# Performance work log

Measured on AMD Instinct MI355X. Metric: run time of the kernel, lower is better.

## Reference

```python
import jax, jax.numpy as jnp
import numpy as np

T, N, D = 4096, 32768, 1024

def setup_inputs() -> dict:
    key = jax.random.key(0)
    k1, k2 = jax.random.split(key)
    x = jax.random.normal(k1, (T, D), dtype=jnp.float32)
    embeddings = jax.random.normal(k2, (N, D), dtype=jnp.float32)
    return {"x": x, "embeddings": embeddings}

def reference(x, embeddings):
    # scores: [T, N] = x @ E^T (unscaled single-head attention, Q=x, K=V=E)
    scores = jnp.einsum('td,nd->tn', x, embeddings)
    probs = jax.nn.softmax(scores, axis=-1)
    # out: [T, D] = probs @ E
    return jnp.einsum('tn,nd->td', probs, embeddings)
```

## Files before the change

kernel.cpp:

```cpp
#include <hip/hip_runtime.h>
#include <stdint.h>

#define T_DIM 4096
#define N_DIM 32768
#define D_DIM 1024
#define QB 64
#define KB 32
#define KSPLIT 4
#define ITERS (N_DIM / KSPLIT / KB)
#define NKB_TOT (N_DIM / KB)

typedef _Float16 f16;
typedef _Float16 f16x8 __attribute__((ext_vector_type(8)));
typedef _Float16 f16x4 __attribute__((ext_vector_type(4)));
typedef float f32x4 __attribute__((ext_vector_type(4)));

#define SWZ(q, k0) ((k0) ^ ((((q) >> 2) & 3) << 2))

struct __align__(16) Lds {
  float Spart[8][64][40];
  f16   P[64][40];
  float srow[64];
};

__global__ void e16_build(const float* __restrict__ E, f16* __restrict__ E16) {
  size_t i8 = (size_t)(blockIdx.x * 256 + threadIdx.x) * 8;
  float4 a = *(const float4*)(E + i8);
  float4 b = *(const float4*)(E + i8 + 4);
  f16x8 v = {(f16)a.x,(f16)a.y,(f16)a.z,(f16)a.w,
             (f16)b.x,(f16)b.y,(f16)b.z,(f16)b.w};
  *(f16x8*)(E16 + i8) = v;
}

__global__ void w2_build(const float* __restrict__ E, f16* __restrict__ W2) {
  int kb = blockIdx.x >> 2;
  int dg = blockIdx.x & 3;
  int d  = dg * 256 + threadIdx.x;
  for (int kq = 0; kq < 4; ++kq) {
    int k0 = kq * 8;
    f16x8 v;
    #pragma unroll
    for (int j = 0; j < 8; ++j)
      v[j] = (f16)E[(size_t)(kb*32 + k0 + j) * D_DIM + d];
    *(f16x8*)(W2 + (size_t)kb * (D_DIM*KB) + (size_t)d*KB + k0) = v;
  }
}

template<int USE_E16>
__global__ __launch_bounds__(512, 2)
void cboe_attn(const float* __restrict__ X, const float* __restrict__ Eg,
               const f16* __restrict__ E16, const f16* __restrict__ W2,
               f16* __restrict__ O16, float* __restrict__ ML)
{
  extern __shared__ char smem_raw[];
  Lds& L = *reinterpret_cast<Lds*>(smem_raw);
  const int tid   = threadIdx.x;
  const int lane  = tid & 63;
  const int w     = tid >> 6;
  const int c     = lane & 15;
  const int g     = lane >> 4;
  const int wd    = w * 128;
  const int qtile = blockIdx.x & 63;
  const int ks    = blockIdx.x >> 6;
  const int qb    = qtile * QB;
  const size_t key0 = (size_t)ks * (N_DIM / KSPLIT);
  const int sq    = tid >> 3;
  const int kslot = tid & 7;

  f16x8 qf[4][4];
  #pragma unroll
  for (int qt = 0; qt < 4; ++qt) {
    const float* qrow = X + (size_t)(qb + qt*16 + c) * D_DIM + wd;
    #pragma unroll
    for (int kc = 0; kc < 4; ++kc) {
      float4 a = *(const float4*)(qrow + kc*32 + g*8);
      float4 b = *(const float4*)(qrow + kc*32 + g*8 + 4);
      qf[qt][kc] = (f16x8){(f16)a.x,(f16)a.y,(f16)a.z,(f16)a.w,
                           (f16)b.x,(f16)b.y,(f16)b.z,(f16)b.w};
    }
  }

  f32x4 acc[4][8];
  #pragma unroll
  for (int qt = 0; qt < 4; ++qt)
    #pragma unroll
    for (int dt = 0; dt < 8; ++dt) acc[qt][dt] = (f32x4){0.f,0.f,0.f,0.f};

  float m_run = -1.0e30f, l_run = 0.0f;

  for (int it = 0; it < ITERS; ++it) {
    const size_t kb_glob = (size_t)ks * ITERS + it;
    const size_t kbase   = key0 + (size_t)it * KB;

    #pragma unroll
    for (int kt = 0; kt < 2; ++kt) {
      const size_t key = kbase + kt*16 + c;
      f16x8 ak[4];
      #pragma unroll
      for (int kc = 0; kc < 4; ++kc) {
        if (USE_E16) {
          ak[kc] = *(const f16x8*)(E16 + key*D_DIM + wd + kc*32 + g*8);
        } else {
          const float* p = Eg + key*D_DIM + wd + kc*32 + g*8;
          float4 a = *(const float4*)p;
          float4 b = *(const float4*)(p + 4);
          ak[kc] = (f16x8){(f16)a.x,(f16)a.y,(f16)a.z,(f16)a.w,
                           (f16)b.x,(f16)b.y,(f16)b.z,(f16)b.w};
        }
      }
      f32x4 sacc[4];
      #pragma unroll
      for (int qt = 0; qt < 4; ++qt) sacc[qt] = (f32x4){0.f,0.f,0.f,0.f};
      #pragma unroll
      for (int kc = 0; kc < 4; ++kc)
        #pragma unroll
        for (int qt = 0; qt < 4; ++qt)
          sacc[qt] = __builtin_amdgcn_mfma_f32_16x16x32_f16(ak[kc], qf[qt][kc], sacc[qt], 0, 0, 0);
      #pragma unroll
      for (int qt = 0; qt < 4; ++qt) {
        int q = qt*16 + c;
        *(f32x4*)&L.Spart[w][q][SWZ(q, kt*16 + g*4)] = sacc[qt];
      }
    }
    __syncthreads();

    f32x4 sv = (f32x4){0.f,0.f,0.f,0.f};
    #pragma unroll
    for (int w8 = 0; w8 < 8; ++w8)
      sv += *(const f32x4*)&L.Spart[w8][sq][SWZ(sq, kslot*4)];
    float tm = fmaxf(fmaxf(sv[0], sv[1]), fmaxf(sv[2], sv[3]));
    tm = fmaxf(tm, __shfl_xor(tm, 1));
    tm = fmaxf(tm, __shfl_xor(tm, 2));
    tm = fmaxf(tm, __shfl_xor(tm, 4));
    float mn = fmaxf(m_run, tm);
    float scale = __expf(m_run - mn);
    float p0 = __expf(sv[0] - mn), p1 = __expf(sv[1] - mn);
    float p2 = __expf(sv[2] - mn), p3 = __expf(sv[3] - mn);
    float psum = (p0 + p1) + (p2 + p3);
    psum += __shfl_xor(psum, 1);
    psum += __shfl_xor(psum, 2);
    psum += __shfl_xor(psum, 4);
    l_run = l_run * scale + psum;
    m_run = mn;
    *(f16x4*)&L.P[sq][kslot*4] = (f16x4){(f16)p0,(f16)p1,(f16)p2,(f16)p3};
    if (kslot == 0) L.srow[sq] = scale;
    __syncthreads();

    #pragma unroll
    for (int qt = 0; qt < 4; ++qt) {
      f32x4 sc = *(const f32x4*)&L.srow[qt*16 + g*4];
      #pragma unroll
      for (int dt = 0; dt < 8; ++dt) {
        acc[qt][dt][0] *= sc[0]; acc[qt][dt][1] *= sc[1];
        acc[qt][dt][2] *= sc[2]; acc[qt][dt][3] *= sc[3];
      }
    }
    f16x8 ap[4];
    #pragma unroll
    for (int qt = 0; qt < 4; ++qt)
      ap[qt] = *(const f16x8*)&L.P[qt*16 + c][g*8];
    const f16* vbase = W2 + kb_glob * (D_DIM*KB);
    #pragma unroll
    for (int dt = 0; dt < 8; ++dt) {
      f16x8 bv = *(const f16x8*)(vbase + (size_t)(wd + dt*16 + c)*KB + g*8);
      #pragma unroll
      for (int qt = 0; qt < 4; ++qt)
        acc[qt][dt] = __builtin_amdgcn_mfma_f32_16x16x32_f16(ap[qt], bv, acc[qt][dt], 0, 0, 0);
    }
  }

  if (kslot == 0) {
    size_t qg = (size_t)qb + sq;
    ML[((size_t)ks * T_DIM + qg) * 2 + 0] = m_run;
    ML[((size_t)ks * T_DIM + qg) * 2 + 1] = l_run;
  }
  #pragma unroll
  for (int qt = 0; qt < 4; ++qt)
    #pragma unroll
    for (int dt = 0; dt < 8; ++dt)
      #pragma unroll
      for (int r = 0; r < 4; ++r)
        O16[((size_t)ks * T_DIM + qb + qt*16 + 4*g + r) * D_DIM + wd + dt*16 + c] =
            (f16)acc[qt][dt][r];
}

__global__ void combine(const f16* __restrict__ O16, const float* __restrict__ ML,
                        float* __restrict__ Out) {
  int q  = blockIdx.x;
  int d0 = threadIdx.x * 4;
  float m[KSPLIT], l[KSPLIT];
  float M = -1.0e30f;
  #pragma unroll
  for (int ks = 0; ks < KSPLIT; ++ks) {
    m[ks] = ML[((size_t)ks * T_DIM + q) * 2 + 0];
    l[ks] = ML[((size_t)ks * T_DIM + q) * 2 + 1];
    M = fmaxf(M, m[ks]);
  }
  float Lsum = 0.f, wk[KSPLIT];
  #pragma unroll
  for (int ks = 0; ks < KSPLIT; ++ks) {
    wk[ks] = __expf(m[ks] - M);
    Lsum += l[ks] * wk[ks];
  }
  float inv = 1.0f / Lsum;
  float o0 = 0.f, o1 = 0.f, o2 = 0.f, o3 = 0.f;
  #pragma unroll
  for (int ks = 0; ks < KSPLIT; ++ks) {
    f16x4 v = *(const f16x4*)(O16 + ((size_t)ks * T_DIM + q) * D_DIM + d0);
    o0 += wk[ks] * (float)v[0];
    o1 += wk[ks] * (float)v[1];
    o2 += wk[ks] * (float)v[2];
    o3 += wk[ks] * (float)v[3];
  }
  float4 o = {o0 * inv, o1 * inv, o2 * inv, o3 * inv};
  *(float4*)(Out + (size_t)q * D_DIM + d0) = o;
}

extern "C" void kernel_launch(void* const* d_in, const int* in_sizes, int n_in,
                              void* d_out, int out_size, void* d_ws, size_t ws_size,
                              hipStream_t stream) {
  const float* X  = (const float*)d_in[0];
  const float* Eg = (const float*)d_in[1];
  float* Out = (float*)d_out;

  const size_t szE16 = (size_t)N_DIM * D_DIM * sizeof(f16);
  const size_t szW2  = (size_t)NKB_TOT * D_DIM * KB * sizeof(f16);
  const size_t szO16 = (size_t)KSPLIT * T_DIM * D_DIM * sizeof(f16);
  const size_t szML  = (size_t)KSPLIT * T_DIM * 2 * sizeof(float);
  const size_t needT1 = szE16 + szW2 + szO16 + szML;
  const int use_e16 = (d_ws && ws_size >= needT1) ? 1 : 0;

  char* p = (char*)d_ws;
  f16* E16 = nullptr;
  if (use_e16) { E16 = (f16*)p; p += szE16; }
  f16*   W2  = (f16*)p;   p += szW2;
  f16*   O16 = (f16*)p;   p += szO16;
  float* ML  = (float*)p;

  w2_build<<<dim3(NKB_TOT * 4), dim3(256), 0, stream>>>(Eg, W2);
  if (use_e16)
    e16_build<<<dim3((N_DIM * D_DIM) / (256 * 8)), dim3(256), 0, stream>>>(Eg, E16);

  const int shmem = (int)sizeof(Lds);
  if (use_e16) {
    hipFuncSetAttribute(reinterpret_cast<const void*>(&cboe_attn<1>),
                        hipFuncAttributeMaxDynamicSharedMemorySize, shmem);
    cboe_attn<1><<<dim3((T_DIM / QB) * KSPLIT), dim3(512), shmem, stream>>>(
        X, Eg, E16, W2, O16, ML);
  } else {
    hipFuncSetAttribute(reinterpret_cast<const void*>(&cboe_attn<0>),
                        hipFuncAttributeMaxDynamicSharedMemorySize, shmem);
    cboe_attn<0><<<dim3((T_DIM / QB) * KSPLIT), dim3(512), shmem, stream>>>(
        X, Eg, nullptr, W2, O16, ML);
  }
  combine<<<dim3(T_DIM), dim3(256), 0, stream>>>(O16, ML, Out);
}
```

Baseline: 1.835 ms.

## Use 1024-thread blocks with split query/D warps and lazy softmax rescaling

The attention kernel now runs 16 warps per block, with each warp covering half the query rows and a 64-wide slice of D, so each warp holds half the accumulators and Q fragments. The online softmax only raises the running max when it grows by more than 8, and the accumulator rescale is skipped when no row changed. Each partial output is normalised by its own l before writing, and combine is adjusted to match. A naive fp32 fallback kernel replaces the template for small workspaces. Together these aim to cut register pressure and per-iteration exp/multiply work, at the cost of more warps sharing each barrier and some fp16 range risk from the lazy max.

```diff
diff --git a/kernel.cpp b/kernel.cpp
--- a/kernel.cpp
+++ b/kernel.cpp
@@ -13,7 +13,9 @@
 typedef _Float16 f16;
 typedef _Float16 f16x8 __attribute__((ext_vector_type(8)));
 typedef _Float16 f16x4 __attribute__((ext_vector_type(4)));
+typedef _Float16 f16x2 __attribute__((ext_vector_type(2)));
 typedef float f32x4 __attribute__((ext_vector_type(4)));
+typedef float f32x2 __attribute__((ext_vector_type(2)));
 
 #define SWZ(q, k0) ((k0) ^ ((((q) >> 2) & 3) << 2))
 
@@ -21,6 +23,7 @@
   float Spart[8][64][40];
   f16   P[64][40];
   float srow[64];
+  float linv[64];
 };
 
 __global__ void e16_build(const float* __restrict__ E, f16* __restrict__ E16) {
@@ -46,142 +49,139 @@
   }
 }
 
-template<int USE_E16>
-__global__ __launch_bounds__(512, 2)
-void cboe_attn(const float* __restrict__ X, const float* __restrict__ Eg,
-               const f16* __restrict__ E16, const f16* __restrict__ W2,
-               f16* __restrict__ O16, float* __restrict__ ML)
+__global__ __launch_bounds__(1024)
+void cboe_attn(const float* __restrict__ X, const f16* __restrict__ E16,
+               const f16* __restrict__ W2, f16* __restrict__ O16,
+               float* __restrict__ ML)
 {
   extern __shared__ char smem_raw[];
   Lds& L = *reinterpret_cast<Lds*>(smem_raw);
-  const int tid   = threadIdx.x;
-  const int lane  = tid & 63;
-  const int w     = tid >> 6;
-  const int c     = lane & 15;
-  const int g     = lane >> 4;
-  const int wd    = w * 128;
+  const int tid  = threadIdx.x;
+  const int lane = tid & 63;
+  const int w    = tid >> 6;
+  const int c    = lane & 15;
+  const int g    = lane >> 4;
+  const int dq   = w & 7;
+  const int qh   = w >> 3;
+  const int wd   = w * 64;
   const int qtile = blockIdx.x & 63;
   const int ks    = blockIdx.x >> 6;
   const int qb    = qtile * QB;
   const size_t key0 = (size_t)ks * (N_DIM / KSPLIT);
-  const int sq    = tid >> 3;
-  const int kslot = tid & 7;
-
-  f16x8 qf[4][4];
-  #pragma unroll
-  for (int qt = 0; qt < 4; ++qt) {
-    const float* qrow = X + (size_t)(qb + qt*16 + c) * D_DIM + wd;
+  const int sq   = tid >> 4;
+  const int kp   = tid & 15;
+
+  f16x8 qf[2][4];
+  #pragma unroll
+  for (int j = 0; j < 2; ++j) {
+    const float* qrow = X + (size_t)(qb + (qh*2 + j)*16 + c) * D_DIM + dq*128;
     #pragma unroll
     for (int kc = 0; kc < 4; ++kc) {
       float4 a = *(const float4*)(qrow + kc*32 + g*8);
       float4 b = *(const float4*)(qrow + kc*32 + g*8 + 4);
-      qf[qt][kc] = (f16x8){(f16)a.x,(f16)a.y,(f16)a.z,(f16)a.w,
-                           (f16)b.x,(f16)b.y,(f16)b.z,(f16)b.w};
-    }
-  }
-
-  f32x4 acc[4][8];
+      qf[j][kc] = (f16x8){(f16)a.x,(f16)a.y,(f16)a.z,(f16)a.w,
+                          (f16)b.x,(f16)b.y,(f16)b.z,(f16)b.w};
+    }
+  }
+
+  f32x4 acc[4][4];
   #pragma unroll
   for (int qt = 0; qt < 4; ++qt)
     #pragma unroll
-    for (int dt = 0; dt < 8; ++dt) acc[qt][dt] = (f32x4){0.f,0.f,0.f,0.f};
+    for (int dt = 0; dt < 4; ++dt) acc[qt][dt] = (f32x4){0.f,0.f,0.f,0.f};
 
   float m_run = -1.0e30f, l_run = 0.0f;
 
   for (int it = 0; it < ITERS; ++it) {
-    const size_t kb_glob = (size_t)ks * ITERS + it;
-    const size_t kbase   = key0 + (size_t)it * KB;
+    const size_t kbase = key0 + (size_t)it * KB;
 
     #pragma unroll
     for (int kt = 0; kt < 2; ++kt) {
-      const size_t key = kbase + kt*16 + c;
       f16x8 ak[4];
       #pragma unroll
+      for (int kc = 0; kc < 4; ++kc)
+        ak[kc] = *(const f16x8*)(E16 + (kbase + kt*16 + c)*D_DIM + dq*128 + kc*32 + g*8);
+      f32x4 s0 = (f32x4){0.f,0.f,0.f,0.f};
+      f32x4 s1 = (f32x4){0.f,0.f,0.f,0.f};
+      #pragma unroll
       for (int kc = 0; kc < 4; ++kc) {
-        if (USE_E16) {
-          ak[kc] = *(const f16x8*)(E16 + key*D_DIM + wd + kc*32 + g*8);
-        } else {
-          const float* p = Eg + key*D_DIM + wd + kc*32 + g*8;
-          float4 a = *(const float4*)p;
-          float4 b = *(const float4*)(p + 4);
-          ak[kc] = (f16x8){(f16)a.x,(f16)a.y,(f16)a.z,(f16)a.w,
-                           (f16)b.x,(f16)b.y,(f16)b.z,(f16)b.w};
-        }
+        s0 = __builtin_amdgcn_mfma_f32_16x16x32_f16(ak[kc], qf[0][kc], s0, 0, 0, 0);
+        s1 = __builtin_amdgcn_mfma_f32_16x16x32_f16(ak[kc], qf[1][kc], s1, 0, 0, 0);
       }
-      f32x4 sacc[4];
-      #pragma unroll
-      for (int qt = 0; qt < 4; ++qt) sacc[qt] = (f32x4){0.f,0.f,0.f,0.f};
-      #pragma unroll
-      for (int kc = 0; kc < 4; ++kc)
-        #pragma unroll
-        for (int qt = 0; qt < 4; ++qt)
-          sacc[qt] = __builtin_amdgcn_mfma_f32_16x16x32_f16(ak[kc], qf[qt][kc], sacc[qt], 0, 0, 0);
-      #pragma unroll
-      for (int qt = 0; qt < 4; ++qt) {
-        int q = qt*16 + c;
-        *(f32x4*)&L.Spart[w][q][SWZ(q, kt*16 + g*4)] = sacc[qt];
-      }
+      const int q0 = (qh*2 + 0)*16 + c;
+      const int q1 = (qh*2 + 1)*16 + c;
+      *(f32x4*)&L.Spart[dq][q0][SWZ(q0, kt*16 + g*4)] = s0;
+      *(f32x4*)&L.Spart[dq][q1][SWZ(q1, kt*16 + g*4)] = s1;
     }
     __syncthreads();
 
-    f32x4 sv = (f32x4){0.f,0.f,0.f,0.f};
-    #pragma unroll
-    for (int w8 = 0; w8 < 8; ++w8)
-      sv += *(const f32x4*)&L.Spart[w8][sq][SWZ(sq, kslot*4)];
-    float tm = fmaxf(fmaxf(sv[0], sv[1]), fmaxf(sv[2], sv[3]));
+    f32x2 sv = (f32x2){0.f, 0.f};
+    #pragma unroll
+    for (int d8 = 0; d8 < 8; ++d8)
+      sv += *(const f32x2*)&L.Spart[d8][sq][SWZ(sq, 2*kp)];
+    float tm = fmaxf(sv[0], sv[1]);
     tm = fmaxf(tm, __shfl_xor(tm, 1));
     tm = fmaxf(tm, __shfl_xor(tm, 2));
     tm = fmaxf(tm, __shfl_xor(tm, 4));
-    float mn = fmaxf(m_run, tm);
-    float scale = __expf(m_run - mn);
+    tm = fmaxf(tm, __shfl_xor(tm, 8));
+    const bool upd = tm > m_run + 8.0f;
+    const float mn = upd ? tm : m_run;
+    const float scale = upd ? __expf(m_run - mn) : 1.0f;
     float p0 = __expf(sv[0] - mn), p1 = __expf(sv[1] - mn);
-    float p2 = __expf(sv[2] - mn), p3 = __expf(sv[3] - mn);
-    float psum = (p0 + p1) + (p2 + p3);
-    psum += __shfl_xor(psum, 1);
-    psum += __shfl_xor(psum, 2);
-    psum += __shfl_xor(psum, 4);
-    l_run = l_run * scale + psum;
+    *(f16x2*)&L.P[sq][2*kp] = (f16x2){(f16)p0, (f16)p1};
+    float ps = p0 + p1;
+    ps += __shfl_xor(ps, 1);
+    ps += __shfl_xor(ps, 2);
+    ps += __shfl_xor(ps, 4);
+    ps += __shfl_xor(ps, 8);
+    l_run = l_run * scale + ps;
     m_run = mn;
-    *(f16x4*)&L.P[sq][kslot*4] = (f16x4){(f16)p0,(f16)p1,(f16)p2,(f16)p3};
-    if (kslot == 0) L.srow[sq] = scale;
+    if (kp == 0) L.srow[sq] = scale;
     __syncthreads();
 
     #pragma unroll
     for (int qt = 0; qt < 4; ++qt) {
       f32x4 sc = *(const f32x4*)&L.srow[qt*16 + g*4];
-      #pragma unroll
-      for (int dt = 0; dt < 8; ++dt) {
-        acc[qt][dt][0] *= sc[0]; acc[qt][dt][1] *= sc[1];
-        acc[qt][dt][2] *= sc[2]; acc[qt][dt][3] *= sc[3];
+      bool need = (sc[0]!=1.f)|(sc[1]!=1.f)|(sc[2]!=1.f)|(sc[3]!=1.f);
+      if (__any(need)) {
+        #pragma unroll
+        for (int dt = 0; dt < 4; ++dt) {
+          acc[qt][dt][0] *= sc[0]; acc[qt][dt][1] *= sc[1];
+          acc[qt][dt][2] *= sc[2]; acc[qt][dt][3] *= sc[3];
+        }
       }
     }
-    f16x8 ap[4];
-    #pragma unroll
-    for (int qt = 0; qt < 4; ++qt)
-      ap[qt] = *(const f16x8*)&L.P[qt*16 + c][g*8];
-    const f16* vbase = W2 + kb_glob * (D_DIM*KB);
-    #pragma unroll
-    for (int dt = 0; dt < 8; ++dt) {
-      f16x8 bv = *(const f16x8*)(vbase + (size_t)(wd + dt*16 + c)*KB + g*8);
-      #pragma unroll
-      for (int qt = 0; qt < 4; ++qt)
-        acc[qt][dt] = __builtin_amdgcn_mfma_f32_16x16x32_f16(ap[qt], bv, acc[qt][dt], 0, 0, 0);
-    }
-  }
-
-  if (kslot == 0) {
+    const f16* vbase = W2 + (key0/KB + it) * (size_t)(D_DIM*KB);
+    f16x8 bv[4];
+    #pragma unroll
+    for (int dt = 0; dt < 4; ++dt)
+      bv[dt] = *(const f16x8*)(vbase + (size_t)(wd + dt*16 + c)*KB + g*8);
+    #pragma unroll
+    for (int qt = 0; qt < 4; ++qt) {
+      f16x8 ap = *(const f16x8*)&L.P[qt*16 + c][g*8];
+      #pragma unroll
+      for (int dt = 0; dt < 4; ++dt)
+        acc[qt][dt] = __builtin_amdgcn_mfma_f32_16x16x32_f16(ap, bv[dt], acc[qt][dt], 0, 0, 0);
+    }
+  }
+
+  if (kp == 0) {
     size_t qg = (size_t)qb + sq;
     ML[((size_t)ks * T_DIM + qg) * 2 + 0] = m_run;
     ML[((size_t)ks * T_DIM + qg) * 2 + 1] = l_run;
-  }
-  #pragma unroll
-  for (int qt = 0; qt < 4; ++qt)
-    #pragma unroll
-    for (int dt = 0; dt < 8; ++dt)
+    L.linv[sq] = 1.0f / l_run;
+  }
+  __syncthreads();
+  #pragma unroll
+  for (int qt = 0; qt < 4; ++qt) {
+    f32x4 li = *(const f32x4*)&L.linv[qt*16 + g*4];
+    #pragma unroll
+    for (int dt = 0; dt < 4; ++dt)
       #pragma unroll
       for (int r = 0; r < 4; ++r)
         O16[((size_t)ks * T_DIM + qb + qt*16 + 4*g + r) * D_DIM + wd + dt*16 + c] =
-            (f16)acc[qt][dt][r];
+            (f16)(acc[qt][dt][r] * li[r]);
+  }
 }
 
 __global__ void combine(const f16* __restrict__ O16, const float* __restrict__ ML,
@@ -196,13 +196,13 @@
     l[ks] = ML[((size_t)ks * T_DIM + q) * 2 + 1];
     M = fmaxf(M, m[ks]);
   }
-  float Lsum = 0.f, wk[KSPLIT];
+  float W = 0.f, wk[KSPLIT];
   #pragma unroll
   for (int ks = 0; ks < KSPLIT; ++ks) {
-    wk[ks] = __expf(m[ks] - M);
-    Lsum += l[ks] * wk[ks];
-  }
-  float inv = 1.0f / Lsum;
+    wk[ks] = l[ks] * __expf(m[ks] - M);
+    W += wk[ks];
+  }
+  float inv = 1.0f / W;
   float o0 = 0.f, o1 = 0.f, o2 = 0.f, o3 = 0.f;
   #pragma unroll
   for (int ks = 0; ks < KSPLIT; ++ks) {
@@ -216,6 +216,38 @@
   *(float4*)(Out + (size_t)q * D_DIM + d0) = o;
 }
 
+__global__ void cboe_naive(const float* __restrict__ X, const float* __restrict__ E,
+                           float* __restrict__ Out) {
+  int row  = blockIdx.x * 4 + (threadIdx.x >> 6);
+  int lane = threadIdx.x & 63;
+  float xq[16], acc[16];
+  #pragma unroll
+  for (int j = 0; j < 16; ++j) {
+    xq[j] = X[(size_t)row * D_DIM + lane*16 + j];
+    acc[j] = 0.f;
+  }
+  float m = -1.0e30f, l = 0.f;
+  for (int key = 0; key < N_DIM; ++key) {
+    const float* er = E + (size_t)key * D_DIM + lane*16;
+    float ev[16];
+    float s = 0.f;
+    #pragma unroll
+    for (int j = 0; j < 16; ++j) { ev[j] = er[j]; s += xq[j] * ev[j]; }
+    #pragma unroll
+    for (int sh = 1; sh < 64; sh <<= 1) s += __shfl_xor(s, sh);
+    float mn = fmaxf(m, s);
+    float sc = __expf(m - mn);
+    float p  = __expf(s - mn);
+    l = l * sc + p;
+    #pragma unroll
+    for (int j = 0; j < 16; ++j) acc[j] = acc[j] * sc + p * ev[j];
+    m = mn;
+  }
+  #pragma unroll
+  for (int j = 0; j < 16; ++j)
+    Out[(size_t)row * D_DIM + lane*16 + j] = acc[j] / l;
+}
+
 extern "C" void kernel_launch(void* const* d_in, const int* in_sizes, int n_in,
                               void* d_out, int out_size, void* d_ws, size_t ws_size,
                               hipStream_t stream) {
@@ -227,31 +259,26 @@
   const size_t szW2  = (size_t)NKB_TOT * D_DIM * KB * sizeof(f16);
   const size_t szO16 = (size_t)KSPLIT * T_DIM * D_DIM * sizeof(f16);
   const size_t szML  = (size_t)KSPLIT * T_DIM * 2 * sizeof(float);
-  const size_t needT1 = szE16 + szW2 + szO16 + szML;
-  const int use_e16 = (d_ws && ws_size >= needT1) ? 1 : 0;
+  const size_t need  = szE16 + szW2 + szO16 + szML;
+
+  if (!d_ws || ws_size < need) {
+    cboe_naive<<<dim3(T_DIM/4), dim3(256), 0, stream>>>(X, Eg, Out);
+    return;
+  }
 
   char* p = (char*)d_ws;
-  f16* E16 = nullptr;
-  if (use_e16) { E16 = (f16*)p; p += szE16; }
+  f16*   E16 = (f16*)p;   p += szE16;
   f16*   W2  = (f16*)p;   p += szW2;
   f16*   O16 = (f16*)p;   p += szO16;
   float* ML  = (float*)p;
 
+  e16_build<<<dim3((N_DIM * D_DIM) / (256 * 8)), dim3(256), 0, stream>>>(Eg, E16);
   w2_build<<<dim3(NKB_TOT * 4), dim3(256), 0, stream>>>(Eg, W2);
-  if (use_e16)
-    e16_build<<<dim3((N_DIM * D_DIM) / (256 * 8)), dim3(256), 0, stream>>>(Eg, E16);
 
   const int shmem = (int)sizeof(Lds);
-  if (use_e16) {
-    hipFuncSetAttribute(reinterpret_cast<const void*>(&cboe_attn<1>),
-                        hipFuncAttributeMaxDynamicSharedMemorySize, shmem);
-    cboe_attn<1><<<dim3((T_DIM / QB) * KSPLIT), dim3(512), shmem, stream>>>(
-        X, Eg, E16, W2, O16, ML);
-  } else {
-    hipFuncSetAttribute(reinterpret_cast<const void*>(&cboe_attn<0>),
-                        hipFuncAttributeMaxDynamicSharedMemorySize, shmem);
-    cboe_attn<0><<<dim3((T_DIM / QB) * KSPLIT), dim3(512), shmem, stream>>>(
-        X, Eg, nullptr, W2, O16, ML);
-  }
+  hipFuncSetAttribute(reinterpret_cast<const void*>(&cboe_attn),
+                      hipFuncAttributeMaxDynamicSharedMemorySize, shmem);
+  cboe_attn<<<dim3((T_DIM / QB) * KSPLIT), dim3(1024), shmem, stream>>>(
+      X, E16, W2, O16, ML);
   combine<<<dim3(T_DIM), dim3(256), 0, stream>>>(O16, ML, Out);
 }
```

Measured after the change: 2.933 ms. 1.6x slower.
